# Optimization experiments

Hardware: AMD Instinct MI355X
Metric: run time of the kernel (lower is better)

Reference implementation:

```python
import jax, jax.numpy as jnp
import numpy as np

GS = 256      # grid/node count
PARAM = 128   # feature width
KC = 32       # keepconst (constant features)
I1, I2 = 64, 32
PK = PARAM - KC
K_DIV = 16.0  # neighbor-count normalizer
EPS = 1e-3    # Keras BatchNorm default epsilon
B = 4


def _bn(x, g, b, m, v):
    # inference-mode batch norm over last axis
    return (x - m) * jax.lax.rsqrt(v + EPS) * g + b


def setup_inputs() -> dict:
    key = jax.random.key(0)
    ks = jax.random.split(key, 24)
    mat = (jax.random.uniform(ks[0], (B, GS, GS)) < (K_DIV / GS)).astype(jnp.float32)
    val = jax.random.normal(ks[1], (B, GS, PARAM), dtype=jnp.float32)
    def w(k, shape):
        fan = shape[0] if len(shape) > 1 else shape[0]
        return jax.random.normal(k, shape, dtype=jnp.float32) * (1.0 / np.sqrt(fan))
    inp = {
        'mat': mat, 'val': val,
        'M1': w(ks[2], (2 * PARAM, I1)), 'B1': 0.05 * jax.random.normal(ks[3], (I1,)),
        'M2': w(ks[4], (I1, I2)),        'B2': 0.05 * jax.random.normal(ks[5], (I2,)),
        'M3': w(ks[6], (I2, PK)),        'B3': 0.05 * jax.random.normal(ks[7], (PK,)),
    }
    for idx, d in zip((1, 2, 3), (I1, I2, PK)):
        kk = jax.random.split(ks[7 + idx], 4)
        inp[f'g{idx}'] = 1.0 + 0.1 * jax.random.normal(kk[0], (d,), dtype=jnp.float32)
        inp[f'b{idx}'] = 0.1 * jax.random.normal(kk[1], (d,), dtype=jnp.float32)
        inp[f'm{idx}'] = 0.1 * jax.random.normal(kk[2], (d,), dtype=jnp.float32)
        inp[f'v{idx}'] = jax.random.uniform(kk[3], (d,), dtype=jnp.float32, minval=0.5, maxval=1.5)
    return inp


def reference(mat, val, M1, B1, M2, B2, M3, B3,
              g1, b1, m1, v1, g2, b2, m2, v2, g3, b3, m3, v3):
    con = val[:, :, :KC]
    # selector matmuls == gather: pair i -> (a=i//GS, b=i%GS)
    feat = jnp.repeat(val, GS, axis=1)          # (B, GS*GS, PARAM) = val_a
    vb = jnp.tile(val, (1, GS, 1))              # (B, GS*GS, PARAM) = val_b
    premlp = jnp.concatenate([feat, vb - feat], axis=-1)  # (B, GS*GS, 2*PARAM)
    s = jax.nn.relu(_bn(premlp @ M1 + B1, g1, b1, m1, v1))
    s = jax.nn.relu(_bn(s @ M2 + B2, g2, b2, m2, v2))
    s = jax.nn.relu(_bn(s @ M3 + B3, g3, b3, m3, v3))      # (B, GS*GS, PK)
    res = s.reshape(val.shape[0], GS, GS, PK)               # (B, a, b, PK)
    # masked scatter-sum over neighbor axis b
    summ = jnp.einsum('babk,bab->bak'.replace('a', 'x').replace('b', 'y', 1), res, mat) if False else \
        jnp.einsum('bxyk,bxy->bxk', res, mat)               # (B, GS, PK)
    var = jnp.clip(summ / K_DIV, -1.0, 1.0)                 # advrelu([-1,1]) == clip
    return jnp.concatenate([con, var], axis=-1)             # (B, GS, PARAM)
```

## Files before the change

kernel.cpp:

```cpp
#include <hip/hip_runtime.h>

#define GS    256
#define PARAM 128
#define KC    32
#define I1    64
#define I2    32
#define PK    96
#define B_    4
#define NROWS (B_ * GS)
#define EPS   1e-3f
#define KDIV_INV (1.0f / 16.0f)

constexpr int U_OFF   = 0;
constexpr int W_OFF   = NROWS * I1;
constexpr int M2F_OFF = 2 * NROWS * I1;
constexpr int C2_OFF  = M2F_OFF + I1 * I2;
constexpr int M3F_OFF = C2_OFF + I2;
constexpr int C3_OFF  = M3F_OFF + I2 * PK;
constexpr int C1_OFF  = C3_OFF + PK;

__device__ __forceinline__ float rdlane(float v, int l) {
    return __uint_as_float(__builtin_amdgcn_readlane(__float_as_uint(v), l));
}

__global__ __launch_bounds__(256) void glmlp_precompute(
    const float* __restrict__ val, const float* __restrict__ M1,
    const float* __restrict__ B1,
    const float* __restrict__ M2, const float* __restrict__ B2,
    const float* __restrict__ M3, const float* __restrict__ B3,
    const float* __restrict__ g1, const float* __restrict__ b1,
    const float* __restrict__ m1, const float* __restrict__ v1,
    const float* __restrict__ g2, const float* __restrict__ b2,
    const float* __restrict__ m2, const float* __restrict__ v2,
    const float* __restrict__ g3, const float* __restrict__ b3,
    const float* __restrict__ m3, const float* __restrict__ v3,
    float* __restrict__ ws, float* __restrict__ out)
{
    const int blk = blockIdx.x;
    const int t = threadIdx.x;

    if (blk < NROWS) {
        __shared__ float vrow[PARAM];
        __shared__ float red[4][I1];
        const int r = blk;
        if (t < PARAM) vrow[t] = val[r * PARAM + t];
        if (t < KC) out[r * PARAM + t] = val[r * PARAM + t];
        __syncthreads();

        const int i = t & (I1 - 1);
        const int q = t >> 6;
        const float* __restrict__ Mb = M1 + ((q >> 1) ? (PARAM * I1) : 0);
        const int p0 = (q & 1) * 64;
        float aa = 0.f, bb = 0.f;
        #pragma unroll 8
        for (int p = 0; p < 64; p += 2) {
            aa = fmaf(vrow[p0 + p],     Mb[(p0 + p) * I1 + i],     aa);
            bb = fmaf(vrow[p0 + p + 1], Mb[(p0 + p + 1) * I1 + i], bb);
        }
        red[q][i] = aa + bb;
        __syncthreads();

        if (q == 0) {
            const float T  = red[0][i] + red[1][i];
            const float Wv = red[2][i] + red[3][i];
            const float s1 = g1[i] * rsqrtf(v1[i] + EPS);
            ws[U_OFF + r * I1 + i] = (T - Wv) * s1;
            ws[W_OFF + r * I1 + i] = Wv * s1;
        }
    } else {
        if (t < I1) {
            const float s1 = g1[t] * rsqrtf(v1[t] + EPS);
            ws[C1_OFF + t] = B1[t] * s1 + b1[t] - m1[t] * s1;
        }
        if (t < I2) {
            const float s2 = g2[t] * rsqrtf(v2[t] + EPS);
            ws[C2_OFF + t] = B2[t] * s2 + b2[t] - m2[t] * s2;
        }
        if (t < PK) {
            const float s3 = g3[t] * rsqrtf(v3[t] + EPS);
            ws[C3_OFF + t] = B3[t] * s3 + b3[t] - m3[t] * s3;
        }
        for (int idx = t; idx < I1 * I2; idx += 256) {
            const int j = idx & (I2 - 1);
            const float s2 = g2[j] * rsqrtf(v2[j] + EPS);
            ws[M2F_OFF + idx] = M2[idx] * s2;
        }
        for (int idx = t; idx < I2 * PK; idx += 256) {
            const int k = idx % PK;
            const float s3 = g3[k] * rsqrtf(v3[k] + EPS);
            ws[M3F_OFF + idx] = M3[idx] * s3;
        }
    }
}

__global__ __launch_bounds__(256) void glmlp_pairs(
    const float* __restrict__ mat, const float* __restrict__ ws,
    float* __restrict__ out)
{
    __shared__ int   acty[GS];
    __shared__ float partial[4][PK];
    __shared__ int   cnt;

    const int r = blockIdx.x;
    const int t = threadIdx.x;
    const int lane = t & 63;
    const int w = t >> 6;
    const int jj = lane & 31;
    const int wbase = r & ~(GS - 1);
    const float* __restrict__ W = ws + W_OFF;

    if (t == 0) cnt = 0;
    const float mv = mat[r * GS + t];

    float m2col[I1];
    #pragma unroll
    for (int s = 0; s < I1; ++s)
        m2col[s] = ws[M2F_OFF + s * I2 + jj];
    float m3a[I2], m3b[I2];
    #pragma unroll
    for (int i = 0; i < I2; ++i) {
        m3a[i] = ws[M3F_OFF + i * PK + lane];
        m3b[i] = ws[M3F_OFF + i * PK + 64 + jj];
    }
    const float ux  = ws[U_OFF + r * I1 + lane] + ws[C1_OFF + lane];
    const float c2j = ws[C2_OFF + jj];
    const float c30 = ws[C3_OFF + lane];
    const float c31 = ws[C3_OFF + 64 + jj];

    __syncthreads();
    if (mv != 0.0f) acty[atomicAdd(&cnt, 1)] = t;
    __syncthreads();
    const int n = cnt;

    float acc0 = 0.f, acc1 = 0.f;

    int p = w;
    float wv = (p < n) ? W[(wbase + acty[p]) * I1 + lane] : 0.f;
    while (p < n) {
        const int pn = p + 4;
        const float wvn = (pn < n) ? W[(wbase + acty[pn]) * I1 + lane] : 0.f;

        const float h1 = fmaxf(ux + wv, 0.f);

        float a0 = 0.f, a1 = 0.f, a2 = 0.f, a3 = 0.f;
        #pragma unroll
        for (int s = 0; s < I1; s += 4) {
            a0 = fmaf(rdlane(h1, s + 0), m2col[s + 0], a0);
            a1 = fmaf(rdlane(h1, s + 1), m2col[s + 1], a1);
            a2 = fmaf(rdlane(h1, s + 2), m2col[s + 2], a2);
            a3 = fmaf(rdlane(h1, s + 3), m2col[s + 3], a3);
        }
        const float h2 = fmaxf((a0 + a1) + (a2 + a3) + c2j, 0.f);

        float d0a = c30, d0b = 0.f, d1a = c31, d1b = 0.f;
        #pragma unroll
        for (int i = 0; i < I2; i += 2) {
            const float he = rdlane(h2, i);
            const float ho = rdlane(h2, i + 1);
            d0a = fmaf(he, m3a[i],     d0a);
            d0b = fmaf(ho, m3a[i + 1], d0b);
            d1a = fmaf(he, m3b[i],     d1a);
            d1b = fmaf(ho, m3b[i + 1], d1b);
        }
        acc0 += fmaxf(d0a + d0b, 0.f);
        acc1 += fmaxf(d1a + d1b, 0.f);

        wv = wvn;
        p = pn;
    }

    partial[w][lane] = acc0;
    if (lane < 32) partial[w][64 + lane] = acc1;
    __syncthreads();

    if (t < PK) {
        float v = (partial[0][t] + partial[1][t] + partial[2][t] + partial[3][t])
                  * KDIV_INV;
        v = fminf(fmaxf(v, -1.0f), 1.0f);
        out[r * PARAM + KC + t] = v;
    }
}

extern "C" void kernel_launch(void* const* d_in, const int* in_sizes, int n_in,
                              void* d_out, int out_size, void* d_ws, size_t ws_size,
                              hipStream_t stream) {
    const float* mat = (const float*)d_in[0];
    const float* val = (const float*)d_in[1];
    const float* M1  = (const float*)d_in[2];
    const float* B1  = (const float*)d_in[3];
    const float* M2  = (const float*)d_in[4];
    const float* B2  = (const float*)d_in[5];
    const float* M3  = (const float*)d_in[6];
    const float* B3  = (const float*)d_in[7];
    const float* g1  = (const float*)d_in[8];
    const float* b1  = (const float*)d_in[9];
    const float* m1  = (const float*)d_in[10];
    const float* v1  = (const float*)d_in[11];
    const float* g2  = (const float*)d_in[12];
    const float* b2  = (const float*)d_in[13];
    const float* m2  = (const float*)d_in[14];
    const float* v2  = (const float*)d_in[15];
    const float* g3  = (const float*)d_in[16];
    const float* b3  = (const float*)d_in[17];
    const float* m3  = (const float*)d_in[18];
    const float* v3  = (const float*)d_in[19];

    float* ws  = (float*)d_ws;
    float* out = (float*)d_out;

    hipLaunchKernelGGL(glmlp_precompute, dim3(NROWS + 1), dim3(256), 0, stream,
                       val, M1, B1, M2, B2, M3, B3,
                       g1, b1, m1, v1, g2, b2, m2, v2, g3, b3, m3, v3,
                       ws, out);

    hipLaunchKernelGGL(glmlp_pairs, dim3(NROWS), dim3(256), 0, stream,
                       mat, ws, out);
}
```

Before: 109.8 us.

## Assign one row per wavefront with ballot-based neighbor enumeration

Each wavefront now processes a whole row instead of four wavefronts splitting one row's neighbors. Neighbor indices come from 64-bit ballots walked with ctz, replacing the shared-memory atomic compaction and the LDS cross-wave reduction. This drops the block barriers and atomics, but per-wave work now depends on each row's neighbor count (about 16) rather than being split four ways, and there are a quarter as many blocks. Each wave still loads the full M2/M3 register weights, now once per row instead of being shared across a row.

```diff
diff --git a/kernel.cpp b/kernel.cpp
--- a/kernel.cpp
+++ b/kernel.cpp
@@ -97,20 +97,17 @@
     const float* __restrict__ mat, const float* __restrict__ ws,
     float* __restrict__ out)
 {
-    __shared__ int   acty[GS];
-    __shared__ float partial[4][PK];
-    __shared__ int   cnt;
-
-    const int r = blockIdx.x;
     const int t = threadIdx.x;
     const int lane = t & 63;
-    const int w = t >> 6;
+    const int r = blockIdx.x * 4 + (t >> 6);
     const int jj = lane & 31;
     const int wbase = r & ~(GS - 1);
     const float* __restrict__ W = ws + W_OFF;
 
-    if (t == 0) cnt = 0;
-    const float mv = mat[r * GS + t];
+    const unsigned long long bal0 = __ballot(mat[r * GS +   0 + lane] != 0.f);
+    const unsigned long long bal1 = __ballot(mat[r * GS +  64 + lane] != 0.f);
+    const unsigned long long bal2 = __ballot(mat[r * GS + 128 + lane] != 0.f);
+    const unsigned long long bal3 = __ballot(mat[r * GS + 192 + lane] != 0.f);
 
     float m2col[I1];
     #pragma unroll
@@ -127,18 +124,28 @@
     const float c30 = ws[C3_OFF + lane];
     const float c31 = ws[C3_OFF + 64 + jj];
 
-    __syncthreads();
-    if (mv != 0.0f) acty[atomicAdd(&cnt, 1)] = t;
-    __syncthreads();
-    const int n = cnt;
+    unsigned long long cur = bal0;
+    int c = 0;
+    auto advance = [&]() -> int {
+        while (cur == 0ULL) {
+            ++c;
+            if (c == 1)      cur = bal1;
+            else if (c == 2) cur = bal2;
+            else if (c == 3) cur = bal3;
+            else             return -1;
+        }
+        const int b = __builtin_ctzll(cur);
+        cur &= cur - 1;
+        return (c << 6) + b;
+    };
 
     float acc0 = 0.f, acc1 = 0.f;
 
-    int p = w;
-    float wv = (p < n) ? W[(wbase + acty[p]) * I1 + lane] : 0.f;
-    while (p < n) {
-        const int pn = p + 4;
-        const float wvn = (pn < n) ? W[(wbase + acty[pn]) * I1 + lane] : 0.f;
+    int y = advance();
+    float wv = (y >= 0) ? W[(wbase + y) * I1 + lane] : 0.f;
+    while (y >= 0) {
+        const int yn = advance();
+        const float wvn = (yn >= 0) ? W[(wbase + yn) * I1 + lane] : 0.f;
 
         const float h1 = fmaxf(ux + wv, 0.f);
 
@@ -165,19 +172,17 @@
         acc0 += fmaxf(d0a + d0b, 0.f);
         acc1 += fmaxf(d1a + d1b, 0.f);
 
+        y = yn;
         wv = wvn;
-        p = pn;
-    }
-
-    partial[w][lane] = acc0;
-    if (lane < 32) partial[w][64 + lane] = acc1;
-    __syncthreads();
-
-    if (t < PK) {
-        float v = (partial[0][t] + partial[1][t] + partial[2][t] + partial[3][t])
-                  * KDIV_INV;
-        v = fminf(fmaxf(v, -1.0f), 1.0f);
-        out[r * PARAM + KC + t] = v;
+    }
+
+    {
+        const float v0 = fminf(fmaxf(acc0 * KDIV_INV, -1.f), 1.f);
+        out[r * PARAM + KC + lane] = v0;
+        if (lane < 32) {
+            const float v1 = fminf(fmaxf(acc1 * KDIV_INV, -1.f), 1.f);
+            out[r * PARAM + KC + 64 + lane] = v1;
+        }
     }
 }
 
@@ -213,6 +218,6 @@
                        g1, b1, m1, v1, g2, b2, m2, v2, g3, b3, m3, v3,
                        ws, out);
 
-    hipLaunchKernelGGL(glmlp_pairs, dim3(NROWS), dim3(256), 0, stream,
+    hipLaunchKernelGGL(glmlp_pairs, dim3(NROWS / 4), dim3(256), 0, stream,
                        mat, ws, out);
 }
```

After: 122.5 us. +11.6%, slower.
